# Optimization experiments

Measured on AMD Instinct MI355X. Metric: run time of the kernel, lower is better.

## Reference

```python
import jax, jax.numpy as jnp
import numpy as np

C = 256       # planes
S = 4         # sub-spectral groups
N, F, T = 16, 64, 256
EPS = 1e-5
WQ = (8, 7)   # weight quant (bits, frac)
AQ = (8, 4)   # activation quant
AQ_SRAM = (8, 4)
BNMQ = (8, 7) # bn scale quant
BNBQ = (8, 4) # bn bias quant


def fixpoint(x, q):
    """Fixed-point quantize to q=(total_bits, frac_bits), straight-through estimator."""
    bits, frac = q
    scale = 2.0 ** frac
    qmax = 2.0 ** (bits - 1) - 1.0
    qmin = -(2.0 ** (bits - 1))
    qx = jnp.clip(jnp.round(x * scale), qmin, qmax) / scale
    return x + jax.lax.stop_gradient(qx - x)


def dwconv(x, w, pad):
    # x: [N,C,H,W], w: [C,1,kh,kw] depthwise (groups=C)
    return jax.lax.conv_general_dilated(
        x, w, window_strides=(1, 1), padding=pad,
        dimension_numbers=('NCHW', 'OIHW', 'NCHW'),
        feature_group_count=x.shape[1])


def qbn(x, gamma, beta, mean, var):
    # quantized inference batchnorm: y = x*m + b with m, b fixed-point
    m = fixpoint(gamma / jnp.sqrt(var + EPS), BNMQ)
    b = fixpoint(beta - mean * m, BNBQ)
    return x * m[None, :, None, None] + b[None, :, None, None]


def setup_inputs() -> dict:
    key = jax.random.key(0)
    ks = jax.random.split(key, 12)
    return {
        'x': jax.random.normal(ks[0], (N, C, F, T), dtype=jnp.float32),
        'w_freq': jax.random.normal(ks[1], (C, 1, 3, 1), dtype=jnp.float32) * 0.2,
        'ssn_gamma': 1.0 + 0.1 * jax.random.normal(ks[2], (C * S,), dtype=jnp.float32),
        'ssn_beta': 0.1 * jax.random.normal(ks[3], (C * S,), dtype=jnp.float32),
        'ssn_mean': 0.1 * jax.random.normal(ks[4], (C * S,), dtype=jnp.float32),
        'ssn_var': jax.random.uniform(ks[5], (C * S,), minval=0.5, maxval=1.5, dtype=jnp.float32),
        'w_temp': jax.random.normal(ks[6], (C, 1, 1, 3), dtype=jnp.float32) * 0.2,
        'bn2_gamma': 1.0 + 0.1 * jax.random.normal(ks[7], (C,), dtype=jnp.float32),
        'bn2_beta': 0.1 * jax.random.normal(ks[8], (C,), dtype=jnp.float32),
        'bn2_mean': 0.1 * jax.random.normal(ks[9], (C,), dtype=jnp.float32),
        'bn2_var': jax.random.uniform(ks[10], (C,), minval=0.5, maxval=1.5, dtype=jnp.float32),
        'w_1x1': jax.random.normal(ks[11], (C, C, 1, 1), dtype=jnp.float32) * 0.06,
    }


def reference(x, w_freq, ssn_gamma, ssn_beta, ssn_mean, ssn_var,
              w_temp, bn2_gamma, bn2_beta, bn2_mean, bn2_var, w_1x1):
    # freq depthwise conv (3,1), pad (1,0), quantized weights
    out = dwconv(x, fixpoint(w_freq, WQ), ((1, 1), (0, 0)))
    out = fixpoint(out, AQ)
    # sub-spectral norm: view [N, C*S, F//S, T], BN, view back
    n, c, f, t = out.shape
    out = out.reshape(n, c * S, f // S, t)
    out = qbn(out, ssn_gamma, ssn_beta, ssn_mean, ssn_var)
    out = out.reshape(n, c, f, t)
    out = fixpoint(out, AQ)
    auxilary = fixpoint(out, AQ_SRAM)
    # mean over freq, keepdim
    out = out.mean(axis=2, keepdims=True)
    out = fixpoint(out, AQ)
    # temporal depthwise conv (1,3), pad (0,1)
    out = dwconv(out, fixpoint(w_temp, WQ), ((0, 0), (1, 1)))
    out = fixpoint(out, AQ)
    out = qbn(out, bn2_gamma, bn2_beta, bn2_mean, bn2_var)
    out = fixpoint(out, AQ)
    out = jax.nn.relu(out)  # 'swish' in source is nn.ReLU()
    out = fixpoint(out, AQ)
    # 1x1 pointwise conv via einsum over channels
    out = jnp.einsum('nchw,oc->nohw', out, fixpoint(w_1x1, WQ)[:, :, 0, 0])
    out = fixpoint(out, AQ)
    out = auxilary + out  # broadcasts over freq dim
    out = fixpoint(out, AQ)
    return jax.nn.relu(out)
```

## Files before the change

### kernel.cpp

```cpp
#include <hip/hip_runtime.h>

#define N_ 16
#define C_ 256
#define F_ 64
#define T_ 256

typedef float f32x4 __attribute__((ext_vector_type(4)));

__device__ __forceinline__ float clampf(float v, float lo, float hi) {
    return fminf(fmaxf(v, lo), hi);
}

__device__ __forceinline__ float qcode(float x, float scale) {
    return clampf(rintf(x * scale), -128.f, 127.f);
}

__global__ __launch_bounds__(256) void aux_mean_kernel(
    const float* __restrict__ x,
    const float* __restrict__ wf,
    const float* __restrict__ ssn_g,
    const float* __restrict__ ssn_b,
    const float* __restrict__ ssn_mu,
    const float* __restrict__ ssn_va,
    signed char* __restrict__ aux_s8,
    signed char* __restrict__ mean_s8)
{
    const int wave = threadIdx.x >> 6;
    const int lane = threadIdx.x & 63;
    const int plane = blockIdx.x * 4 + wave;
    const int c = plane & (C_ - 1);
    const int t0 = lane * 4;

    const f32x4* xp = (const f32x4*)(x + (size_t)plane * (F_ * T_) + t0);
    signed char*  ap = aux_s8 + (size_t)plane * (F_ * T_) + t0;

    const float w0 = qcode(wf[c * 3 + 0], 128.f) * (1.f / 128.f);
    const float w1 = qcode(wf[c * 3 + 1], 128.f) * (1.f / 128.f);
    const float w2 = qcode(wf[c * 3 + 2], 128.f) * (1.f / 128.f);

    f32x4 xm; xm.x = 0.f; xm.y = 0.f; xm.z = 0.f; xm.w = 0.f;
    f32x4 x0 = xp[0];
    int s0 = 0, s1 = 0, s2 = 0, s3 = 0;

    int f = 0;
    for (int g = 0; g < 4; ++g) {
        const int cs = c * 4 + g;
        const float m  = qcode(ssn_g[cs] * rsqrtf(ssn_va[cs] + 1e-5f), 128.f) * (1.f / 128.f);
        const float bc = qcode(ssn_b[cs] - ssn_mu[cs] * m, 16.f);
        #pragma unroll 8
        for (int fi = 0; fi < 16; ++fi, ++f) {
            f32x4 xn;
            if (f < F_ - 1) xn = xp[(f + 1) * (T_ / 4)];
            else            { xn.x = 0.f; xn.y = 0.f; xn.z = 0.f; xn.w = 0.f; }

            float ka0, ka1, ka2, ka3;
            {
                float conv = xm.x * w0 + x0.x * w1 + xn.x * w2;
                float q1c = clampf(rintf(conv * 16.f), -128.f, 127.f);
                ka0 = clampf(rintf(fmaf(q1c, m, bc)), -128.f, 127.f);
            }
            {
                float conv = xm.y * w0 + x0.y * w1 + xn.y * w2;
                float q1c = clampf(rintf(conv * 16.f), -128.f, 127.f);
                ka1 = clampf(rintf(fmaf(q1c, m, bc)), -128.f, 127.f);
            }
            {
                float conv = xm.z * w0 + x0.z * w1 + xn.z * w2;
                float q1c = clampf(rintf(conv * 16.f), -128.f, 127.f);
                ka2 = clampf(rintf(fmaf(q1c, m, bc)), -128.f, 127.f);
            }
            {
                float conv = xm.w * w0 + x0.w * w1 + xn.w * w2;
                float q1c = clampf(rintf(conv * 16.f), -128.f, 127.f);
                ka3 = clampf(rintf(fmaf(q1c, m, bc)), -128.f, 127.f);
            }
            const int i0 = (int)ka0, i1 = (int)ka1, i2 = (int)ka2, i3 = (int)ka3;
            s0 += i0; s1 += i1; s2 += i2; s3 += i3;
            char4 cv;
            cv.x = (signed char)i0; cv.y = (signed char)i1;
            cv.z = (signed char)i2; cv.w = (signed char)i3;
            *(char4*)(ap + f * T_) = cv;

            xm = x0; x0 = xn;
        }
    }

    char4 mv;
    mv.x = (signed char)(int)clampf(rintf((float)s0 * (1.f / 64.f)), -128.f, 127.f);
    mv.y = (signed char)(int)clampf(rintf((float)s1 * (1.f / 64.f)), -128.f, 127.f);
    mv.z = (signed char)(int)clampf(rintf((float)s2 * (1.f / 64.f)), -128.f, 127.f);
    mv.w = (signed char)(int)clampf(rintf((float)s3 * (1.f / 64.f)), -128.f, 127.f);
    *(char4*)(mean_s8 + (size_t)plane * T_ + t0) = mv;
}

#define TT_ 16
#define ZP_ (TT_ + 4)
__global__ __launch_bounds__(256) void mean_path_kernel(
    const signed char* __restrict__ mean_s8,
    const float* __restrict__ wt,
    const float* __restrict__ g2,
    const float* __restrict__ b2,
    const float* __restrict__ mu2,
    const float* __restrict__ va2,
    const float* __restrict__ w1,
    signed char* __restrict__ y_s8)
{
    const int n = blockIdx.x >> 4;
    const int tt = (blockIdx.x & 15) * TT_;
    const int tid = threadIdx.x;

    __shared__ float z[C_][ZP_];

    {
        const int c = tid;
        const float wq0 = qcode(wt[c * 3 + 0], 128.f) * (1.f / 128.f);
        const float wq1 = qcode(wt[c * 3 + 1], 128.f) * (1.f / 128.f);
        const float wq2 = qcode(wt[c * 3 + 2], 128.f) * (1.f / 128.f);
        const float m2 = qcode(g2[c] * rsqrtf(va2[c] + 1e-5f), 128.f) * (1.f / 128.f);
        const float bc2 = qcode(b2[c] - mu2[c] * m2, 16.f);
        const signed char* mp = mean_s8 + (n * C_ + c) * T_;
        #pragma unroll
        for (int j = 0; j < TT_; ++j) {
            const int t = tt + j;
            const float a    = (t > 0)      ? (float)mp[t - 1] : 0.f;
            const float bmid =                (float)mp[t];
            const float d    = (t < T_ - 1) ? (float)mp[t + 1] : 0.f;
            float tcc = a * wq0 + bmid * wq1 + d * wq2;
            float q1c = clampf(rintf(tcc), -128.f, 127.f);
            float v   = clampf(rintf(fmaf(q1c, m2, bc2)), -128.f, 127.f);
            v = fmaxf(v, 0.f);
            z[c][j] = v * (1.f / 16.f);
        }
    }
    __syncthreads();
    {
        const int o = tid;
        float acc[TT_];
        #pragma unroll
        for (int j = 0; j < TT_; ++j) acc[j] = 0.f;
        const float* wrow = w1 + o * C_;
        for (int c = 0; c < C_; c += 4) {
            const f32x4 wv4 = *(const f32x4*)(wrow + c);
            const float wq[4] = {
                qcode(wv4.x, 128.f) * (1.f / 128.f),
                qcode(wv4.y, 128.f) * (1.f / 128.f),
                qcode(wv4.z, 128.f) * (1.f / 128.f),
                qcode(wv4.w, 128.f) * (1.f / 128.f)
            };
            #pragma unroll
            for (int u = 0; u < 4; ++u) {
                const float wv = wq[u];
                const f32x4 za = *(const f32x4*)&z[c + u][0];
                const f32x4 zb = *(const f32x4*)&z[c + u][4];
                const f32x4 zc = *(const f32x4*)&z[c + u][8];
                const f32x4 zd = *(const f32x4*)&z[c + u][12];
                acc[0]  += za.x * wv; acc[1]  += za.y * wv; acc[2]  += za.z * wv; acc[3]  += za.w * wv;
                acc[4]  += zb.x * wv; acc[5]  += zb.y * wv; acc[6]  += zb.z * wv; acc[7]  += zb.w * wv;
                acc[8]  += zc.x * wv; acc[9]  += zc.y * wv; acc[10] += zc.z * wv; acc[11] += zc.w * wv;
                acc[12] += zd.x * wv; acc[13] += zd.y * wv; acc[14] += zd.z * wv; acc[15] += zd.w * wv;
            }
        }
        signed char* yp = y_s8 + (n * C_ + o) * T_ + tt;
        #pragma unroll
        for (int j = 0; j < TT_; ++j) {
            yp[j] = (signed char)(int)qcode(acc[j], 16.f);
        }
    }
}

__global__ __launch_bounds__(256) void combine_kernel(
    const signed char* __restrict__ aux_s8,
    const signed char* __restrict__ y_s8,
    float* __restrict__ out)
{
    const int wave = threadIdx.x >> 6;
    const int lane = threadIdx.x & 63;
    const int plane = blockIdx.x * 4 + wave;
    const int t0 = lane * 4;

    const char4 yk = *(const char4*)(y_s8 + (size_t)plane * T_ + t0);
    const int y0 = yk.x, y1 = yk.y, y2 = yk.z, y3 = yk.w;

    const char4* ap = (const char4*)(aux_s8 + (size_t)plane * (F_ * T_) + t0);
    f32x4* op = (f32x4*)(out + (size_t)plane * (F_ * T_) + t0);

    #pragma unroll 8
    for (int f = 0; f < F_; ++f) {
        const char4 ak = ap[f * (T_ / 4)];
        const int o0 = min(127, max(0, (int)ak.x + y0));
        const int o1 = min(127, max(0, (int)ak.y + y1));
        const int o2 = min(127, max(0, (int)ak.z + y2));
        const int o3 = min(127, max(0, (int)ak.w + y3));
        f32x4 ov;
        ov.x = (float)o0 * (1.f / 16.f);
        ov.y = (float)o1 * (1.f / 16.f);
        ov.z = (float)o2 * (1.f / 16.f);
        ov.w = (float)o3 * (1.f / 16.f);
        op[f * (T_ / 4)] = ov;
    }
}

extern "C" void kernel_launch(void* const* d_in, const int* in_sizes, int n_in,
                              void* d_out, int out_size, void* d_ws, size_t ws_size,
                              hipStream_t stream) {
    const float* x       = (const float*)d_in[0];
    const float* w_freq  = (const float*)d_in[1];
    const float* ssn_g   = (const float*)d_in[2];
    const float* ssn_b   = (const float*)d_in[3];
    const float* ssn_mu  = (const float*)d_in[4];
    const float* ssn_va  = (const float*)d_in[5];
    const float* w_temp  = (const float*)d_in[6];
    const float* g2      = (const float*)d_in[7];
    const float* b2      = (const float*)d_in[8];
    const float* mu2     = (const float*)d_in[9];
    const float* va2     = (const float*)d_in[10];
    const float* w_1x1   = (const float*)d_in[11];
    float* out = (float*)d_out;

    signed char* aux_s8  = (signed char*)d_ws;
    signed char* mean_s8 = aux_s8 + (size_t)N_ * C_ * F_ * T_;
    signed char* y_s8    = mean_s8 + (size_t)N_ * C_ * T_;

    dim3 blk(256);
    aux_mean_kernel<<<dim3(N_ * C_ / 4), blk, 0, stream>>>(
        x, w_freq, ssn_g, ssn_b, ssn_mu, ssn_va, aux_s8, mean_s8);
    mean_path_kernel<<<dim3(N_ * (T_ / TT_)), blk, 0, stream>>>(
        mean_s8, w_temp, g2, b2, mu2, va2, w_1x1, y_s8);
    combine_kernel<<<dim3(N_ * C_ / 4), blk, 0, stream>>>(
        aux_s8, y_s8, out);
}
```

Before: 526.4 us.

## Fuse all stages into one cooperative kernel with grid sync, keeping aux in registers

Replaces the three-kernel pipeline with a single cooperative kernel. Each wave computes the freq conv, SSN and quantized activations for its plane and holds them in 64 packed registers instead of writing an int8 aux tensor to global memory. It computes the temporal conv and BN2 in place using shuffles, writes a small int8 z tensor, does a grid-wide sync, then runs the 1x1 conv per output channel and writes the final output. This removes the aux round trip and two launches, but it needs all 1024 blocks resident at once and puts heavy register pressure on auxq[64]. If the cooperative launch fails, the code falls back to the old three-kernel path.

```diff
diff --git a/kernel.cpp b/kernel.cpp
--- a/kernel.cpp
+++ b/kernel.cpp
@@ -1,4 +1,7 @@
 #include <hip/hip_runtime.h>
+#include <hip/hip_cooperative_groups.h>
+
+namespace cg = cooperative_groups;
 
 #define N_ 16
 #define C_ 256
@@ -13,6 +16,177 @@
 
 __device__ __forceinline__ float qcode(float x, float scale) {
     return clampf(rintf(x * scale), -128.f, 127.f);
+}
+
+__global__ __launch_bounds__(256, 4) void fused_kernel(
+    const float* __restrict__ x,
+    const float* __restrict__ wf,
+    const float* __restrict__ ssn_g,
+    const float* __restrict__ ssn_b,
+    const float* __restrict__ ssn_mu,
+    const float* __restrict__ ssn_va,
+    const float* __restrict__ wt,
+    const float* __restrict__ g2,
+    const float* __restrict__ b2,
+    const float* __restrict__ mu2,
+    const float* __restrict__ va2,
+    const float* __restrict__ w1,
+    signed char* __restrict__ zt,
+    float* __restrict__ out)
+{
+    const int wave = threadIdx.x >> 6;
+    const int lane = threadIdx.x & 63;
+    const int plane = blockIdx.x * 4 + wave;
+    const int c = plane & (C_ - 1);
+    const int n = plane >> 8;
+    const int t0 = lane * 4;
+
+    __shared__ float wq_l[4][C_];
+
+    {
+        const int w = threadIdx.x >> 6;
+        const int j = (threadIdx.x & 63) * 4;
+        const int crow = (blockIdx.x * 4 + w) & (C_ - 1);
+        const f32x4 wv = *(const f32x4*)(w1 + crow * C_ + j);
+        wq_l[w][j + 0] = qcode(wv.x, 128.f);
+        wq_l[w][j + 1] = qcode(wv.y, 128.f);
+        wq_l[w][j + 2] = qcode(wv.z, 128.f);
+        wq_l[w][j + 3] = qcode(wv.w, 128.f);
+    }
+    __syncthreads();
+
+    const f32x4* xp = (const f32x4*)(x + (size_t)plane * (F_ * T_) + t0);
+
+    const float w0 = qcode(wf[c * 3 + 0], 128.f) * (1.f / 128.f);
+    const float w1c = qcode(wf[c * 3 + 1], 128.f) * (1.f / 128.f);
+    const float w2 = qcode(wf[c * 3 + 2], 128.f) * (1.f / 128.f);
+
+    int auxq[F_];
+    f32x4 xm; xm.x = 0.f; xm.y = 0.f; xm.z = 0.f; xm.w = 0.f;
+    f32x4 x0 = xp[0];
+    int s0 = 0, s1 = 0, s2 = 0, s3 = 0;
+
+    #pragma unroll
+    for (int g = 0; g < 4; ++g) {
+        const int cs = c * 4 + g;
+        const float m  = qcode(ssn_g[cs] * rsqrtf(ssn_va[cs] + 1e-5f), 128.f) * (1.f / 128.f);
+        const float bc = qcode(ssn_b[cs] - ssn_mu[cs] * m, 16.f);
+        #pragma unroll
+        for (int fi = 0; fi < 16; ++fi) {
+            const int f = g * 16 + fi;
+            f32x4 xn;
+            if (f < F_ - 1) xn = xp[(f + 1) * (T_ / 4)];
+            else            { xn.x = 0.f; xn.y = 0.f; xn.z = 0.f; xn.w = 0.f; }
+
+            float ka0, ka1, ka2, ka3;
+            {
+                float conv = xm.x * w0 + x0.x * w1c + xn.x * w2;
+                float q1c = clampf(rintf(conv * 16.f), -128.f, 127.f);
+                ka0 = clampf(rintf(fmaf(q1c, m, bc)), -128.f, 127.f);
+            }
+            {
+                float conv = xm.y * w0 + x0.y * w1c + xn.y * w2;
+                float q1c = clampf(rintf(conv * 16.f), -128.f, 127.f);
+                ka1 = clampf(rintf(fmaf(q1c, m, bc)), -128.f, 127.f);
+            }
+            {
+                float conv = xm.z * w0 + x0.z * w1c + xn.z * w2;
+                float q1c = clampf(rintf(conv * 16.f), -128.f, 127.f);
+                ka2 = clampf(rintf(fmaf(q1c, m, bc)), -128.f, 127.f);
+            }
+            {
+                float conv = xm.w * w0 + x0.w * w1c + xn.w * w2;
+                float q1c = clampf(rintf(conv * 16.f), -128.f, 127.f);
+                ka3 = clampf(rintf(fmaf(q1c, m, bc)), -128.f, 127.f);
+            }
+            const int i0 = (int)ka0, i1 = (int)ka1, i2 = (int)ka2, i3 = (int)ka3;
+            s0 += i0; s1 += i1; s2 += i2; s3 += i3;
+            auxq[f] = (i0 & 255) | ((i1 & 255) << 8) | ((i2 & 255) << 16) | (i3 << 24);
+            xm = x0; x0 = xn;
+        }
+    }
+
+    const float m0 = clampf(rintf((float)s0 * (1.f / 64.f)), -128.f, 127.f);
+    const float m1 = clampf(rintf((float)s1 * (1.f / 64.f)), -128.f, 127.f);
+    const float m2v = clampf(rintf((float)s2 * (1.f / 64.f)), -128.f, 127.f);
+    const float m3 = clampf(rintf((float)s3 * (1.f / 64.f)), -128.f, 127.f);
+
+    float left  = __shfl_up(m3, 1);   if (lane == 0)  left  = 0.f;
+    float right = __shfl_down(m0, 1); if (lane == 63) right = 0.f;
+    {
+        const float tw0 = qcode(wt[c * 3 + 0], 128.f) * (1.f / 128.f);
+        const float tw1 = qcode(wt[c * 3 + 1], 128.f) * (1.f / 128.f);
+        const float tw2 = qcode(wt[c * 3 + 2], 128.f) * (1.f / 128.f);
+        const float mm2 = qcode(g2[c] * rsqrtf(va2[c] + 1e-5f), 128.f) * (1.f / 128.f);
+        const float bb2 = qcode(b2[c] - mu2[c] * mm2, 16.f);
+
+        float zc[4];
+        const float a0 = left,  b0 = m0,  d0 = m1;
+        const float a1 = m0,    b1 = m1,  d1 = m2v;
+        const float a2 = m1,    b2_ = m2v, d2 = m3;
+        const float a3 = m2v,   b3 = m3,  d3 = right;
+        {
+            float tcc = a0 * tw0 + b0 * tw1 + d0 * tw2;
+            float q1c = clampf(rintf(tcc), -128.f, 127.f);
+            zc[0] = fmaxf(clampf(rintf(fmaf(q1c, mm2, bb2)), -128.f, 127.f), 0.f);
+        }
+        {
+            float tcc = a1 * tw0 + b1 * tw1 + d1 * tw2;
+            float q1c = clampf(rintf(tcc), -128.f, 127.f);
+            zc[1] = fmaxf(clampf(rintf(fmaf(q1c, mm2, bb2)), -128.f, 127.f), 0.f);
+        }
+        {
+            float tcc = a2 * tw0 + b2_ * tw1 + d2 * tw2;
+            float q1c = clampf(rintf(tcc), -128.f, 127.f);
+            zc[2] = fmaxf(clampf(rintf(fmaf(q1c, mm2, bb2)), -128.f, 127.f), 0.f);
+        }
+        {
+            float tcc = a3 * tw0 + b3 * tw1 + d3 * tw2;
+            float q1c = clampf(rintf(tcc), -128.f, 127.f);
+            zc[3] = fmaxf(clampf(rintf(fmaf(q1c, mm2, bb2)), -128.f, 127.f), 0.f);
+        }
+        const int z0 = (int)zc[0], z1 = (int)zc[1], z2 = (int)zc[2], z3 = (int)zc[3];
+        *(int*)(zt + (size_t)plane * T_ + t0) =
+            (z0 & 255) | ((z1 & 255) << 8) | ((z2 & 255) << 16) | (z3 << 24);
+    }
+
+    __threadfence();
+    cg::this_grid().sync();
+
+    float ya0 = 0.f, ya1 = 0.f, ya2 = 0.f, ya3 = 0.f;
+    {
+        const signed char* zrow = zt + ((size_t)n * C_) * T_ + t0;
+        const float* wqr = &wq_l[wave][0];
+        #pragma unroll 8
+        for (int cc = 0; cc < C_; ++cc) {
+            const float wv = wqr[cc];
+            const int u = *(const int*)(zrow + cc * T_);
+            ya0 += wv * (float)(signed char)(u);
+            ya1 += wv * (float)(signed char)(u >> 8);
+            ya2 += wv * (float)(signed char)(u >> 16);
+            ya3 += wv * (float)(u >> 24);
+        }
+    }
+    const int iy0 = (int)clampf(rintf(ya0 * (1.f / 128.f)), -128.f, 127.f);
+    const int iy1 = (int)clampf(rintf(ya1 * (1.f / 128.f)), -128.f, 127.f);
+    const int iy2 = (int)clampf(rintf(ya2 * (1.f / 128.f)), -128.f, 127.f);
+    const int iy3 = (int)clampf(rintf(ya3 * (1.f / 128.f)), -128.f, 127.f);
+
+    f32x4* op = (f32x4*)(out + (size_t)plane * (F_ * T_) + t0);
+    #pragma unroll
+    for (int f = 0; f < F_; ++f) {
+        const int u = auxq[f];
+        const int o0 = min(127, max(0, ((int)(signed char)(u))       + iy0));
+        const int o1 = min(127, max(0, ((int)(signed char)(u >> 8))  + iy1));
+        const int o2 = min(127, max(0, ((int)(signed char)(u >> 16)) + iy2));
+        const int o3 = min(127, max(0, (u >> 24)                     + iy3));
+        f32x4 ov;
+        ov.x = (float)o0 * (1.f / 16.f);
+        ov.y = (float)o1 * (1.f / 16.f);
+        ov.z = (float)o2 * (1.f / 16.f);
+        ov.w = (float)o3 * (1.f / 16.f);
+        op[f * (T_ / 4)] = ov;
+    }
 }
 
 __global__ __launch_bounds__(256) void aux_mean_kernel(
@@ -52,7 +226,6 @@
             f32x4 xn;
             if (f < F_ - 1) xn = xp[(f + 1) * (T_ / 4)];
             else            { xn.x = 0.f; xn.y = 0.f; xn.z = 0.f; xn.w = 0.f; }
-
             float ka0, ka1, ka2, ka3;
             {
                 float conv = xm.x * w0 + x0.x * w1 + xn.x * w2;
@@ -80,11 +253,9 @@
             cv.x = (signed char)i0; cv.y = (signed char)i1;
             cv.z = (signed char)i2; cv.w = (signed char)i3;
             *(char4*)(ap + f * T_) = cv;
-
             xm = x0; x0 = xn;
         }
     }
-
     char4 mv;
     mv.x = (signed char)(int)clampf(rintf((float)s0 * (1.f / 64.f)), -128.f, 127.f);
     mv.y = (signed char)(int)clampf(rintf((float)s1 * (1.f / 64.f)), -128.f, 127.f);
@@ -108,9 +279,7 @@
     const int n = blockIdx.x >> 4;
     const int tt = (blockIdx.x & 15) * TT_;
     const int tid = threadIdx.x;
-
     __shared__ float z[C_][ZP_];
-
     {
         const int c = tid;
         const float wq0 = qcode(wt[c * 3 + 0], 128.f) * (1.f / 128.f);
@@ -139,8 +308,8 @@
         #pragma unroll
         for (int j = 0; j < TT_; ++j) acc[j] = 0.f;
         const float* wrow = w1 + o * C_;
-        for (int c = 0; c < C_; c += 4) {
-            const f32x4 wv4 = *(const f32x4*)(wrow + c);
+        for (int cbase = 0; cbase < C_; cbase += 4) {
+            const f32x4 wv4 = *(const f32x4*)(wrow + cbase);
             const float wq[4] = {
                 qcode(wv4.x, 128.f) * (1.f / 128.f),
                 qcode(wv4.y, 128.f) * (1.f / 128.f),
@@ -150,10 +319,10 @@
             #pragma unroll
             for (int u = 0; u < 4; ++u) {
                 const float wv = wq[u];
-                const f32x4 za = *(const f32x4*)&z[c + u][0];
-                const f32x4 zb = *(const f32x4*)&z[c + u][4];
-                const f32x4 zc = *(const f32x4*)&z[c + u][8];
-                const f32x4 zd = *(const f32x4*)&z[c + u][12];
+                const f32x4 za = *(const f32x4*)&z[cbase + u][0];
+                const f32x4 zb = *(const f32x4*)&z[cbase + u][4];
+                const f32x4 zc = *(const f32x4*)&z[cbase + u][8];
+                const f32x4 zd = *(const f32x4*)&z[cbase + u][12];
                 acc[0]  += za.x * wv; acc[1]  += za.y * wv; acc[2]  += za.z * wv; acc[3]  += za.w * wv;
                 acc[4]  += zb.x * wv; acc[5]  += zb.y * wv; acc[6]  += zb.z * wv; acc[7]  += zb.w * wv;
                 acc[8]  += zc.x * wv; acc[9]  += zc.y * wv; acc[10] += zc.z * wv; acc[11] += zc.w * wv;
@@ -217,15 +386,27 @@
     const float* w_1x1   = (const float*)d_in[11];
     float* out = (float*)d_out;
 
-    signed char* aux_s8  = (signed char*)d_ws;
+    signed char* zt      = (signed char*)d_ws;
+    signed char* aux_s8  = (signed char*)d_ws + (size_t)(1 << 20);
     signed char* mean_s8 = aux_s8 + (size_t)N_ * C_ * F_ * T_;
     signed char* y_s8    = mean_s8 + (size_t)N_ * C_ * T_;
 
-    dim3 blk(256);
-    aux_mean_kernel<<<dim3(N_ * C_ / 4), blk, 0, stream>>>(
-        x, w_freq, ssn_g, ssn_b, ssn_mu, ssn_va, aux_s8, mean_s8);
-    mean_path_kernel<<<dim3(N_ * (T_ / TT_)), blk, 0, stream>>>(
-        mean_s8, w_temp, g2, b2, mu2, va2, w_1x1, y_s8);
-    combine_kernel<<<dim3(N_ * C_ / 4), blk, 0, stream>>>(
-        aux_s8, y_s8, out);
-}
+    void* args[] = {
+        (void*)&x, (void*)&w_freq, (void*)&ssn_g, (void*)&ssn_b,
+        (void*)&ssn_mu, (void*)&ssn_va, (void*)&w_temp, (void*)&g2,
+        (void*)&b2, (void*)&mu2, (void*)&va2, (void*)&w_1x1,
+        (void*)&zt, (void*)&out
+    };
+    hipError_t err = hipLaunchCooperativeKernel(
+        (const void*)fused_kernel, dim3(N_ * C_ / 4), dim3(256), args, 0, stream);
+
+    if (err != hipSuccess) {
+        dim3 blk(256);
+        aux_mean_kernel<<<dim3(N_ * C_ / 4), blk, 0, stream>>>(
+            x, w_freq, ssn_g, ssn_b, ssn_mu, ssn_va, aux_s8, mean_s8);
+        mean_path_kernel<<<dim3(N_ * (T_ / TT_)), blk, 0, stream>>>(
+            mean_s8, w_temp, g2, b2, mu2, va2, w_1x1, y_s8);
+        combine_kernel<<<dim3(N_ * C_ / 4), blk, 0, stream>>>(
+            aux_s8, y_s8, out);
+    }
+}
```

Result: slower. 859.4 us (+63.3%).
